# Optimization experiments

Measured on AMD Instinct MI355X. Metric: run time of the kernel, lower is better.

## Reference

```python
import jax, jax.numpy as jnp
import numpy as np

COMMITMENT_COST = 0.25

def _conv(x, w, stride, pad):
    return jax.lax.conv_general_dilated(
        x, w, window_strides=(stride, stride),
        padding=((pad, pad), (pad, pad)),
        dimension_numbers=("NCHW", "OIHW", "NCHW"))

def _gelu(x):
    return jax.nn.gelu(x, approximate=False)

def setup_inputs() -> dict:
    key = jax.random.key(0)
    ks = jax.random.split(key, 9)
    def w(k, shape):
        fan_in = shape[1] * shape[2] * shape[3]
        return jax.random.normal(k, shape, jnp.float32) / jnp.sqrt(fan_in)
    return {
        "x": jax.random.normal(ks[0], (32, 3, 256, 256), jnp.float32),
        "enc_w1": w(ks[1], (64, 3, 5, 5)),
        "enc_w2": w(ks[2], (64, 64, 5, 5)),
        "enc_w3": w(ks[3], (64, 64, 2, 2)),
        "dec_w1": w(ks[4], (512, 64, 2, 2)),
        "dec_w2": w(ks[5], (256, 512, 2, 2)),
        "dec_w3": w(ks[6], (256, 256, 2, 2)),
        "codes": jax.random.normal(ks[7], (24, 64), jnp.float32),
        "ema_count": jax.random.uniform(ks[8], (24,), jnp.float32) + 0.1,
    }

def reference(x, enc_w1, enc_w2, enc_w3, dec_w1, dec_w2, dec_w3, codes, ema_count):
    # ---- encoder: 256 -> 128 -> 64 -> 63, channels 3 -> 64 ----
    z = _conv(x, enc_w1, 2, 2)
    z = _gelu(z)
    z = _conv(z, enc_w2, 2, 2)
    z = _gelu(z)
    z = _conv(z, enc_w3, 1, 0)          # [B, 64, 63, 63]

    # ---- VQ codebook (EMA variant: commitment loss only) ----
    B, C, H, W = z.shape
    zf = jnp.transpose(z, (0, 2, 3, 1)).reshape(-1, C)          # [N, C]
    # squared L2 distances to each code
    d = (jnp.sum(zf * zf, axis=1, keepdims=True)
         - 2.0 * zf @ codes.T
         + jnp.sum(codes * codes, axis=1))                       # [N, K]
    idx = jnp.argmin(d, axis=1)                                  # [N]
    zq = codes[idx].reshape(B, H, W, C).transpose(0, 3, 1, 2)    # [B, C, H, W]

    vq_loss = COMMITMENT_COST * jnp.mean(
        (jax.lax.stop_gradient(zq) - z) ** 2)
    # straight-through estimator
    z_hat = z + jax.lax.stop_gradient(zq - z)

    # code probabilities from EMA cluster counts, gathered per position
    probs = ema_count / jnp.sum(ema_count)                       # [K]
    z_probs = probs[idx].reshape(B, H, W)                        # [B, H, W]

    # ---- decoder: 63 -> 64 -> 63 -> 64, channels 64 -> 512 -> 256 -> 256 ----
    y = _conv(z_hat, dec_w1, 1, 1)
    y = _gelu(y)
    y = _conv(y, dec_w2, 1, 0)
    y = _gelu(y)
    x_hat = _conv(y, dec_w3, 1, 1)      # [B, 256, 64, 64]

    return (x_hat, z_probs, vq_loss)
```

## Files before the change

kernel.cpp:

```cpp
#include <hip/hip_runtime.h>
#include <hip/hip_bf16.h>


#define DEV_INLINE __device__ __forceinline__

typedef __attribute__((ext_vector_type(8))) short bf16x8;
typedef __attribute__((ext_vector_type(4))) float f32x4;

#define GLL16(g, l) __builtin_amdgcn_global_load_lds(                      \
    (const __attribute__((address_space(1))) void*)(g),                    \
    (__attribute__((address_space(3))) void*)(l), 16, 0, 0)

DEV_INLINE float gelu_exact(float v) {
    return 0.5f * v * (1.0f + erff(v * 0.70710678118654752440f));
}

__global__ void wtf_k(const float* __restrict__ w, float* __restrict__ wt,
                      int C, int total) {
    int t = blockIdx.x * 256 + threadIdx.x;
    if (t >= total) return;
    int oc = t & 63;
    int rest = t >> 6;
    int tap = rest % 25, c = rest / 25;
    wt[t] = w[(oc * C + c) * 25 + tap];
}

template<int C, int IH, int IW>
__global__ __launch_bounds__(256) void conv5s2_t(
    const float* __restrict__ xg,
    const float* __restrict__ wt,
    float* __restrict__ outg) {
    constexpr int OH = IH / 2, OW = IW / 2;
    __shared__ float xin[35 * 36];
    __shared__ float wl[1600];
    const int tid = threadIdx.x;
    const int n = blockIdx.z;
    const int OY0 = blockIdx.y * 16, OX0 = blockIdx.x * 16;
    const int IY0 = OY0 * 2 - 2, IX0 = OX0 * 2 - 2;
    const int og = tid & 3;
    const int pg = tid >> 2;
    const int py = (pg >> 3) * 2, px = (pg & 7) * 2;
    const int ry = py * 2, rx = px * 2;

    f32x4 a00 = {0,0,0,0}, a01 = a00, a02 = a00, a03 = a00;
    f32x4 a10 = a00, a11 = a00, a12 = a00, a13 = a00;
    f32x4 a20 = a00, a21 = a00, a22 = a00, a23 = a00;
    f32x4 a30 = a00, a31 = a00, a32 = a00, a33 = a00;

    const float* xn = xg + (size_t)n * C * IH * IW;
    for (int c = 0; c < C; ++c) {
        {
            const float4* wsrc = (const float4*)(wt + c * 1600);
            float4* wdst = (float4*)wl;
            wdst[tid] = wsrc[tid];
            if (tid < 144) wdst[256 + tid] = wsrc[256 + tid];
        }
        const float* zc = xn + (size_t)c * IH * IW;
        for (int i = tid; i < 1225; i += 256) {
            int r = i / 35, cl = i - r * 35;
            int iy = IY0 + r, ix = IX0 + cl;
            float v = 0.f;
            if ((unsigned)iy < (unsigned)IH && (unsigned)ix < (unsigned)IW)
                v = zc[(size_t)iy * IW + ix];
            xin[r * 36 + cl] = v;
        }
        __syncthreads();
#pragma unroll
        for (int ky = 0; ky < 5; ++ky) {
            const float* r0 = xin + (ry + ky) * 36 + rx;
            const float* r1 = r0 + 72;
#pragma unroll
            for (int kx = 0; kx < 5; ++kx) {
                const f32x4* wq = (const f32x4*)(wl + (ky * 5 + kx) * 64 + og * 16);
                f32x4 w0 = wq[0], w1 = wq[1], w2 = wq[2], w3 = wq[3];
                float xA = r0[kx], xB = r0[kx + 2];
                float xC = r1[kx], xD = r1[kx + 2];
                a00 += xA * w0; a01 += xA * w1; a02 += xA * w2; a03 += xA * w3;
                a10 += xB * w0; a11 += xB * w1; a12 += xB * w2; a13 += xB * w3;
                a20 += xC * w0; a21 += xC * w1; a22 += xC * w2; a23 += xC * w3;
                a30 += xD * w0; a31 += xD * w1; a32 += xD * w2; a33 += xD * w3;
            }
        }
        __syncthreads();
    }
    const int ocb = og * 16;
#define CSTORE(v, oy, ox, q) {                                                \
        float* o = outg + (((size_t)n * 64 + ocb + (q) * 4) * OH + (oy)) * OW \
                   + (ox);                                                    \
        o[0]               = gelu_exact((v).x);                               \
        o[(size_t)OH * OW]     = gelu_exact((v).y);                           \
        o[(size_t)2 * OH * OW] = gelu_exact((v).z);                           \
        o[(size_t)3 * OH * OW] = gelu_exact((v).w); }
    CSTORE(a00, OY0 + py,     OX0 + px,     0); CSTORE(a01, OY0 + py,     OX0 + px,     1);
    CSTORE(a02, OY0 + py,     OX0 + px,     2); CSTORE(a03, OY0 + py,     OX0 + px,     3);
    CSTORE(a10, OY0 + py,     OX0 + px + 1, 0); CSTORE(a11, OY0 + py,     OX0 + px + 1, 1);
    CSTORE(a12, OY0 + py,     OX0 + px + 1, 2); CSTORE(a13, OY0 + py,     OX0 + px + 1, 3);
    CSTORE(a20, OY0 + py + 1, OX0 + px,     0); CSTORE(a21, OY0 + py + 1, OX0 + px,     1);
    CSTORE(a22, OY0 + py + 1, OX0 + px,     2); CSTORE(a23, OY0 + py + 1, OX0 + px,     3);
    CSTORE(a30, OY0 + py + 1, OX0 + px + 1, 0); CSTORE(a31, OY0 + py + 1, OX0 + px + 1, 1);
    CSTORE(a32, OY0 + py + 1, OX0 + px + 1, 2); CSTORE(a33, OY0 + py + 1, OX0 + px + 1, 3);
#undef CSTORE
}

template<int C, int IH, int IW>
__global__ __launch_bounds__(256) void conv5s2_p(
    const float* __restrict__ xg,
    const float* __restrict__ wt,
    float* __restrict__ outg) {
    constexpr int OH = IH / 2, OW = IW / 2;
    __shared__ float xp[2 * 700];
    __shared__ float wl[1600];
    const int tid = threadIdx.x;
    const int n = blockIdx.z;
    const int OY0 = blockIdx.y * 16, OX0 = blockIdx.x * 16;
    const int IY0 = OY0 * 2 - 2, IX0 = OX0 * 2 - 2;
    const int og = tid & 7;
    const int pg = tid >> 3;
    const int py = (pg >> 2) * 2, px = (pg & 3) * 4;
    const int ry = py * 2;
    const int s4 = og & 4;

    f32x4 a000 = {0,0,0,0}, a001 = a000, a010 = a000, a011 = a000;
    f32x4 a020 = a000, a021 = a000, a030 = a000, a031 = a000;
    f32x4 a100 = a000, a101 = a000, a110 = a000, a111 = a000;
    f32x4 a120 = a000, a121 = a000, a130 = a000, a131 = a000;

    const float* xn = xg + (size_t)n * C * IH * IW;
    for (int c = 0; c < C; ++c) {
        {
            const float4* wsrc = (const float4*)(wt + c * 1600);
            float4* wdst = (float4*)wl;
            wdst[tid ^ ((tid >> 3) & 1)] = wsrc[tid];
            if (tid < 144) {
                int i2 = 256 + tid;
                wdst[i2 ^ ((i2 >> 3) & 1)] = wsrc[i2];
            }
        }
        const float* zc = xn + (size_t)c * IH * IW;
        for (int i = tid; i < 1225; i += 256) {
            int r = i / 35, cl = i - r * 35;
            int iy = IY0 + r, ix = IX0 + cl;
            float v = 0.f;
            if ((unsigned)iy < (unsigned)IH && (unsigned)ix < (unsigned)IW)
                v = zc[(size_t)iy * IW + ix];
            xp[(cl & 1) * 700 + r * 20 + (cl >> 1)] = v;
        }
        __syncthreads();

#define PICK8(Ea, Eb, i) ((i) < 4 ? (Ea)[(i) & 3] : (Eb)[(i) & 3])
#define XV(R, kx, jj) (((kx) & 1)                                           \
        ? PICK8(O##R##0, O##R##1, (jj) + ((kx) >> 1))                       \
        : PICK8(E##R##0, E##R##1, (jj) + ((kx) >> 1)))

#pragma unroll
        for (int ky = 0; ky < 5; ++ky) {
            const int R0 = ry + ky;
            const int R1 = R0 + 2;
            const f32x4 E00 = *(const f32x4*)(xp + R0 * 20 + px);
            const f32x4 E01 = *(const f32x4*)(xp + R0 * 20 + px + 4);
            const f32x4 O00 = *(const f32x4*)(xp + 700 + R0 * 20 + px);
            const f32x4 O01 = *(const f32x4*)(xp + 700 + R0 * 20 + px + 4);
            const f32x4 E10 = *(const f32x4*)(xp + R1 * 20 + px);
            const f32x4 E11 = *(const f32x4*)(xp + R1 * 20 + px + 4);
            const f32x4 O10 = *(const f32x4*)(xp + 700 + R1 * 20 + px);
            const f32x4 O11 = *(const f32x4*)(xp + 700 + R1 * 20 + px + 4);
#pragma unroll
            for (int kx = 0; kx < 5; ++kx) {
                const float* wb = wl + (ky * 5 + kx) * 64 + og * 8;
                f32x4 w0 = *(const f32x4*)(wb + s4);
                f32x4 w1 = *(const f32x4*)(wb + (s4 ^ 4));
                float xA = XV(0, kx, 0), xB = XV(0, kx, 1);
                float xC = XV(0, kx, 2), xD = XV(0, kx, 3);
                float xE = XV(1, kx, 0), xF = XV(1, kx, 1);
                float xG = XV(1, kx, 2), xH = XV(1, kx, 3);
                a000 += xA * w0; a001 += xA * w1;
                a010 += xB * w0; a011 += xB * w1;
                a020 += xC * w0; a021 += xC * w1;
                a030 += xD * w0; a031 += xD * w1;
                a100 += xE * w0; a101 += xE * w1;
                a110 += xF * w0; a111 += xF * w1;
                a120 += xG * w0; a121 += xG * w1;
                a130 += xH * w0; a131 += xH * w1;
            }
        }
#undef XV
#undef PICK8
        __syncthreads();
    }

    const size_t HW = (size_t)OH * OW;
#define STR(q, vA, vB, vC, vD, vE, vF, vG, vH) {                           \
        _Pragma("unroll")                                                  \
        for (int j = 0; j < 4; ++j) {                                      \
            float* o = outg + ((size_t)n * 64 + og * 8 + (q) * 4 + j) * HW \
                       + (size_t)(OY0 + py) * OW + (OX0 + px);             \
            f32x4 t0, t1;                                                  \
            t0[0] = gelu_exact((vA)[j]); t0[1] = gelu_exact((vB)[j]);      \
            t0[2] = gelu_exact((vC)[j]); t0[3] = gelu_exact((vD)[j]);      \
            t1[0] = gelu_exact((vE)[j]); t1[1] = gelu_exact((vF)[j]);      \
            t1[2] = gelu_exact((vG)[j]); t1[3] = gelu_exact((vH)[j]);      \
            *(f32x4*)o = t0;                                               \
            *(f32x4*)(o + OW) = t1;                                        \
        } }
    STR(0, a000, a010, a020, a030, a100, a110, a120, a130)
    STR(1, a001, a011, a021, a031, a101, a111, a121, a131)
#undef STR
}

__global__ void conv3_k(const float* __restrict__ z2,
                        const float* __restrict__ w,
                        float* __restrict__ z) {
    __shared__ float wl[1024];
    const int oc0 = blockIdx.y * 4;
    for (int i = threadIdx.x; i < 1024; i += 256) {
        int j = i & 3, r = i >> 2;
        wl[i] = w[(oc0 + j) * 256 + r];
    }
    __syncthreads();
    const int s = blockIdx.x * 256 + threadIdx.x;
    if (s >= 3969) return;
    const int n = blockIdx.z;
    const int oy = s / 63, ox = s % 63;
    const float4* wv = (const float4*)wl;
    float a0 = 0.f, a1 = 0.f, a2 = 0.f, a3 = 0.f;
    const float* zn = z2 + n * 64 * 4096;
    for (int c = 0; c < 64; ++c) {
        const float* zc = zn + c * 4096;
#pragma unroll
        for (int tap = 0; tap < 4; ++tap) {
            int iy = oy + (tap >> 1), ix = ox + (tap & 1);
            float xv = zc[iy * 64 + ix];
            float4 wq = wv[c * 4 + tap];
            a0 += xv * wq.x; a1 += xv * wq.y; a2 += xv * wq.z; a3 += xv * wq.w;
        }
    }
    int obase = (n * 64 + oc0) * 3969 + s;
    z[obase]            = a0;
    z[obase + 3969]     = a1;
    z[obase + 2 * 3969] = a2;
    z[obase + 3 * 3969] = a3;
}

__global__ void vq_k(const float* __restrict__ z,
                     const float* __restrict__ codes,
                     const float* __restrict__ ema,
                     int* __restrict__ idxO,
                     float* __restrict__ zprobsO,
                     float* __restrict__ lossO) {
    __shared__ float cl[1536];
    __shared__ float cn[24];
    __shared__ float pr[24];
    for (int i = threadIdx.x; i < 1536; i += 256) cl[i] = codes[i];
    if (threadIdx.x < 24) pr[threadIdx.x] = ema[threadIdx.x];
    __syncthreads();
    if (threadIdx.x < 24) {
        float sm = 0.f;
        for (int c = 0; c < 64; ++c) { float v = cl[threadIdx.x * 64 + c]; sm += v * v; }
        cn[threadIdx.x] = sm;
    }
    __syncthreads();
    int t = blockIdx.x * 256 + threadIdx.x;
    float l = 0.f;
    if (t < 127008) {
        int b = t / 3969, s = t - b * 3969;
        const float* zp = z + (b * 64) * 3969 + s;
        float zv[64];
        float zn = 0.f;
#pragma unroll
        for (int c = 0; c < 64; ++c) { float v = zp[c * 3969]; zv[c] = v; zn += v * v; }
        float best = 1e30f; int bi = 0;
        for (int k = 0; k < 24; ++k) {
            float dot = 0.f;
#pragma unroll
            for (int c = 0; c < 64; ++c) dot += zv[c] * cl[k * 64 + c];
            float d = zn - 2.f * dot + cn[k];
            if (d < best) { best = d; bi = k; }
        }
        idxO[t] = bi;
        float psum = 0.f;
        for (int k = 0; k < 24; ++k) psum += pr[k];
        zprobsO[t] = pr[bi] / psum;
        for (int c = 0; c < 64; ++c) { float dd = cl[bi * 64 + c] - zv[c]; l += dd * dd; }
    }
    for (int off = 32; off; off >>= 1) l += __shfl_down(l, off, 64);
    if ((threadIdx.x & 63) == 0) atomicAdd(lossO, l);
}

__global__ void dtab_k(const float* __restrict__ codes,
                       const float* __restrict__ w1,
                       float* __restrict__ D) {
    int t = blockIdx.x * 256 + threadIdx.x;
    if (t >= 24 * 4 * 512) return;
    int oc = t & 511, tap = (t >> 9) & 3, k = t >> 11;
    float acc = 0.f;
    for (int c = 0; c < 64; ++c)
        acc += codes[k * 64 + c] * w1[oc * 256 + c * 4 + tap];
    D[t] = acc;
}

__global__ void wt_k(const float* __restrict__ w, __hip_bfloat16* __restrict__ wT,
                     int cl2, int total) {
    int t = blockIdx.x * 256 + threadIdx.x;
    if (t >= total) return;
    int c = t & ((1 << cl2) - 1);
    int tap = (t >> cl2) & 3;
    int oc = t >> (cl2 + 2);
    wT[t] = __float2bfloat16(w[((oc << cl2) + c) * 4 + tap]);
}

__global__ void dec1_k(const int* __restrict__ idx,
                       const float* __restrict__ D,
                       __hip_bfloat16* __restrict__ y1) {
    const int pos = blockIdx.x;
    const int n = pos >> 12, rem = pos & 4095;
    const int iy = rem >> 6, ix = rem & 63;
    const int* idn = idx + n * 3969;
    const int t = threadIdx.x;
    float ax = 0.f, ay = 0.f;
#pragma unroll
    for (int tap = 0; tap < 4; ++tap) {
        int py = iy - 1 + (tap >> 1), px = ix - 1 + (tap & 1);
        if ((unsigned)py < 63u && (unsigned)px < 63u) {
            int k = idn[py * 63 + px];
            float2 v = ((const float2*)(D + (k * 4 + tap) * 512))[t];
            ax += v.x; ay += v.y;
        }
    }
    __hip_bfloat162 o;
    o.x = __float2bfloat16(gelu_exact(ax));
    o.y = __float2bfloat16(gelu_exact(ay));
    ((__hip_bfloat162*)(y1 + (size_t)pos * 512))[t] = o;
}

__global__ __launch_bounds__(256) void dec2_mfma(
    const __hip_bfloat16* __restrict__ y1,
    const __hip_bfloat16* __restrict__ wT,
    const __hip_bfloat16* __restrict__ zp,
    __hip_bfloat16* __restrict__ y2)
{
    __shared__ __hip_bfloat16 As[128 * 32];
    __shared__ __hip_bfloat16 Bs[128 * 32];
    const int tid = threadIdx.x;
    const int wave = tid >> 6, lane = tid & 63;
    const int quad = lane >> 4, l15 = lane & 15;
    const int m0 = blockIdx.x * 128;
    const int oc0 = blockIdx.y * 128;
    const int sub = tid & 3;

    const char* pA[2];
    const char* pB[2];
#pragma unroll
    for (int j = 0; j < 2; ++j) {
        int slot = j * 64 + (tid >> 2);
        int pp = m0 + slot;
        if (pp < 127008) {
            int n = pp / 3969; int r = pp - n * 3969;
            int oy = r / 63;  int ox = r - oy * 63;
            pA[j] = (const char*)y1 + (size_t)((n * 64 + oy) * 64 + ox) * 1024 + sub * 16;
        } else {
            pA[j] = (const char*)zp;
        }
        pB[j] = (const char*)wT + (size_t)(oc0 + slot) * 4096 + sub * 16;
    }
    char* ldsA[2] = {(char*)As + wave * 1024, (char*)As + 4096 + wave * 1024};
    char* ldsB[2] = {(char*)Bs + wave * 1024, (char*)Bs + 4096 + wave * 1024};

    f32x4 acc[4][4] = {};
    const int wm = (wave & 1) * 64;
    const int wn = (wave >> 1) * 64;

#pragma unroll
    for (int tap = 0; tap < 4; ++tap) {
        const int toff = ((tap >> 1) * 64 + (tap & 1)) * 1024;
        for (int kk = 0; kk < 16; ++kk) {
            const int cb = kk * 64;
            GLL16(pA[0] + toff + cb, ldsA[0]);
            GLL16(pA[1] + toff + cb, ldsA[1]);
            GLL16(pB[0] + tap * 1024 + cb, ldsB[0]);
            GLL16(pB[1] + tap * 1024 + cb, ldsB[1]);
            __syncthreads();
            bf16x8 af[4], bf[4];
#pragma unroll
            for (int mi = 0; mi < 4; ++mi)
                af[mi] = *(const bf16x8*)((const char*)As + (wm + mi * 16 + l15) * 64 + quad * 16);
#pragma unroll
            for (int ni = 0; ni < 4; ++ni)
                bf[ni] = *(const bf16x8*)((const char*)Bs + (wn + ni * 16 + l15) * 64 + quad * 16);
#pragma unroll
            for (int mi = 0; mi < 4; ++mi)
#pragma unroll
                for (int ni = 0; ni < 4; ++ni)
                    acc[mi][ni] = __builtin_amdgcn_mfma_f32_16x16x32_bf16(
                        af[mi], bf[ni], acc[mi][ni], 0, 0, 0);
            __syncthreads();
        }
    }
#pragma unroll
    for (int mi = 0; mi < 4; ++mi)
#pragma unroll
        for (int r = 0; r < 4; ++r) {
            int pos = m0 + wm + mi * 16 + quad * 4 + r;
            if (pos < 127008) {
#pragma unroll
                for (int ni = 0; ni < 4; ++ni) {
                    int oc = oc0 + wn + ni * 16 + l15;
                    y2[(size_t)pos * 256 + oc] =
                        __float2bfloat16(gelu_exact(acc[mi][ni][r]));
                }
            }
        }
}

__global__ __launch_bounds__(256) void dec3_mfma(
    const __hip_bfloat16* __restrict__ y2,
    const __hip_bfloat16* __restrict__ wT,
    const __hip_bfloat16* __restrict__ zp,
    float* __restrict__ out)
{
    __shared__ __hip_bfloat16 As[128 * 32];
    __shared__ __hip_bfloat16 Bs[128 * 32];
    const int tid = threadIdx.x;
    const int wave = tid >> 6, lane = tid & 63;
    const int quad = lane >> 4, l15 = lane & 15;
    const int p0 = blockIdx.x * 128;
    const int oc0 = blockIdx.y * 128;
    const int sub = tid & 3;

    const char* pW[2];
    const char* pP[4][2];
#pragma unroll
    for (int j = 0; j < 2; ++j) {
        int slot = j * 64 + (tid >> 2);
        pW[j] = (const char*)wT + (size_t)(oc0 + slot) * 2048 + sub * 16;
        int pp = p0 + slot;
        int n = pp >> 12, rem = pp & 4095;
        int OY = rem >> 6, OX = rem & 63;
#pragma unroll
        for (int tap = 0; tap < 4; ++tap) {
            int iy = OY - 1 + (tap >> 1), ix = OX - 1 + (tap & 1);
            if ((unsigned)iy < 63u && (unsigned)ix < 63u)
                pP[tap][j] = (const char*)y2 + (size_t)(n * 3969 + iy * 63 + ix) * 512 + sub * 16;
            else
                pP[tap][j] = (const char*)zp;
        }
    }
    char* ldsA[2] = {(char*)As + wave * 1024, (char*)As + 4096 + wave * 1024};
    char* ldsB[2] = {(char*)Bs + wave * 1024, (char*)Bs + 4096 + wave * 1024};

    f32x4 acc[4][4] = {};
    const int wm = (wave & 1) * 64;
    const int wn = (wave >> 1) * 64;

#pragma unroll
    for (int tap = 0; tap < 4; ++tap) {
        for (int kk = 0; kk < 8; ++kk) {
            const int cb = kk * 64;
            GLL16(pW[0] + tap * 512 + cb, ldsA[0]);
            GLL16(pW[1] + tap * 512 + cb, ldsA[1]);
            GLL16(pP[tap][0] + cb, ldsB[0]);
            GLL16(pP[tap][1] + cb, ldsB[1]);
            __syncthreads();
            bf16x8 af[4], bf[4];
#pragma unroll
            for (int mi = 0; mi < 4; ++mi)
                af[mi] = *(const bf16x8*)((const char*)As + (wm + mi * 16 + l15) * 64 + quad * 16);
#pragma unroll
            for (int ni = 0; ni < 4; ++ni)
                bf[ni] = *(const bf16x8*)((const char*)Bs + (wn + ni * 16 + l15) * 64 + quad * 16);
#pragma unroll
            for (int mi = 0; mi < 4; ++mi)
#pragma unroll
                for (int ni = 0; ni < 4; ++ni)
                    acc[mi][ni] = __builtin_amdgcn_mfma_f32_16x16x32_bf16(
                        af[mi], bf[ni], acc[mi][ni], 0, 0, 0);
            __syncthreads();
        }
    }
    const int n = p0 >> 12;
    const int posLocal0 = (p0 & 4095) + wn;
#pragma unroll
    for (int mi = 0; mi < 4; ++mi)
#pragma unroll
        for (int r = 0; r < 4; ++r) {
            int oc = oc0 + wm + mi * 16 + quad * 4 + r;
            float* orow = out + ((size_t)(n * 256 + oc) << 12);
#pragma unroll
            for (int ni = 0; ni < 4; ++ni)
                orow[posLocal0 + ni * 16 + l15] = acc[mi][ni][r];
        }
}

__global__ void loss_k(const float* __restrict__ lossO, float* __restrict__ out) {
    out[0] = 0.25f * lossO[0] / 8128512.0f;
}

extern "C" void kernel_launch(void* const* d_in, const int* in_sizes, int n_in,
                              void* d_out, int out_size, void* d_ws, size_t ws_size,
                              hipStream_t stream) {
    const float* x     = (const float*)d_in[0];
    const float* ew1   = (const float*)d_in[1];
    const float* ew2   = (const float*)d_in[2];
    const float* ew3   = (const float*)d_in[3];
    const float* dw1   = (const float*)d_in[4];
    const float* dw2   = (const float*)d_in[5];
    const float* dw3   = (const float*)d_in[6];
    const float* codes = (const float*)d_in[7];
    const float* ema   = (const float*)d_in[8];
    float* out = (float*)d_out;

    char* ws = (char*)d_ws;
    float* z1   = (float*)(ws + 0);
    float* z2   = (float*)(ws + 134217728);
    float* z    = (float*)(ws + 167772160);
    int*   idx  = (int*)  (ws + 200286208);
    float* loss = (float*)(ws + 200794240);
    __hip_bfloat16* zp  = (__hip_bfloat16*)(ws + 200794496);
    float* D    = (float*)(ws + 200864128);
    __hip_bfloat16* wT2 = (__hip_bfloat16*)(ws + 201650560);
    __hip_bfloat16* wT3 = (__hip_bfloat16*)(ws + 202699136);
    float* wt2f = (float*)(ws + 201650560);
    float* wt1f = (float*)(ws + 202699136);
    __hip_bfloat16* y1  = (__hip_bfloat16*)(ws + 0);
    __hip_bfloat16* y2  = (__hip_bfloat16*)(ws + 134217728);

    hipMemsetAsync(loss, 0, 4, stream);
    hipMemsetAsync(zp, 0, 69632, stream);

    wtf_k<<<dim3(19), 256, 0, stream>>>(ew1, wt1f, 3, 4800);
    wtf_k<<<dim3(400), 256, 0, stream>>>(ew2, wt2f, 64, 102400);
    conv5s2_t<3, 256, 256><<<dim3(8, 8, 32), 256, 0, stream>>>(x, wt1f, z1);
    conv5s2_p<64, 128, 128><<<dim3(4, 4, 32), 256, 0, stream>>>(z1, wt2f, z2);
    conv3_k<<<dim3(16, 16, 32), 256, 0, stream>>>(z2, ew3, z);
    vq_k<<<dim3(497), 256, 0, stream>>>(z, codes, ema, idx, out + 33554432, loss);
    dtab_k<<<dim3(192), 256, 0, stream>>>(codes, dw1, D);
    wt_k<<<dim3(2048), 256, 0, stream>>>(dw2, wT2, 9, 524288);
    wt_k<<<dim3(1024), 256, 0, stream>>>(dw3, wT3, 8, 262144);
    dec1_k<<<dim3(131072), 256, 0, stream>>>(idx, D, y1);
    dec2_mfma<<<dim3(993, 2), 256, 0, stream>>>(y1, wT2, zp, y2);
    dec3_mfma<<<dim3(1024, 2), 256, 0, stream>>>(y2, wT3, zp, out);
    loss_k<<<1, 1, 0, stream>>>(loss, out + 33681440);
}
```

Measured before the change: 1.209 ms.

## Double-buffer input and weight tiles in second encoder conv with register prefetch

The second 5x5 stride-2 encoder convolution now keeps two LDS buffers for input patches and weights. It prefetches the next channel's data into registers while computing the current channel, then writes it to the other buffer, so each channel needs one barrier instead of two. Interior tiles use vectorised float2 loads with precomputed offsets in place of per-element bounds checks. This costs double the shared memory, a launch bound that allows one block per SM, and more registers held across the compute loop.

Result: slower. 1.268 ms (+4.8%).

```diff
diff --git a/kernel.cpp b/kernel.cpp
--- a/kernel.cpp
+++ b/kernel.cpp
@@ -103,13 +103,13 @@
 }
 
 template<int C, int IH, int IW>
-__global__ __launch_bounds__(256) void conv5s2_p(
+__global__ __launch_bounds__(256, 1) void conv5s2_p2(
     const float* __restrict__ xg,
     const float* __restrict__ wt,
     float* __restrict__ outg) {
     constexpr int OH = IH / 2, OW = IW / 2;
-    __shared__ float xp[2 * 700];
-    __shared__ float wl[1600];
+    __shared__ float xp[2][1400];
+    __shared__ float wl[2][1600];
     const int tid = threadIdx.x;
     const int n = blockIdx.z;
     const int OY0 = blockIdx.y * 16, OX0 = blockIdx.x * 16;
@@ -120,53 +120,118 @@
     const int ry = py * 2;
     const int s4 = og & 4;
 
+    const bool interior = (IY0 >= 0) && (IY0 + 35 <= IH) &&
+                          (IX0 >= 0) && (IX0 + 36 <= IW);
+
+    const bool hasB = (tid < 59);
+    const int rA = tid / 9,         qA = tid - rA * 9;
+    const int sB = 256 + tid;
+    const int rB = sB / 9,          qB = sB - rB * 9;
+    int gA0, gA1, gA2, gA3, gB0 = 0, gB1 = 0, gB2 = 0, gB3 = 0;
+    int bA0, bA1, bA2, bA3, bB0 = 0, bB1 = 0, bB2 = 0, bB3 = 0;
+    {
+        int iy = IY0 + rA; int rok = ((unsigned)iy < (unsigned)IH);
+        int ixb = IX0 + 4 * qA; int base = iy * IW + ixb;
+        bA0 = rok && ((unsigned)(ixb)     < (unsigned)IW); gA0 = bA0 ? base     : 0;
+        bA1 = rok && ((unsigned)(ixb + 1) < (unsigned)IW); gA1 = bA1 ? base + 1 : 0;
+        bA2 = rok && ((unsigned)(ixb + 2) < (unsigned)IW); gA2 = bA2 ? base + 2 : 0;
+        bA3 = rok && ((unsigned)(ixb + 3) < (unsigned)IW); gA3 = bA3 ? base + 3 : 0;
+        if (interior) gA0 = base;
+    }
+    if (hasB) {
+        int iy = IY0 + rB; int rok = ((unsigned)iy < (unsigned)IH);
+        int ixb = IX0 + 4 * qB; int base = iy * IW + ixb;
+        bB0 = rok && ((unsigned)(ixb)     < (unsigned)IW); gB0 = bB0 ? base     : 0;
+        bB1 = rok && ((unsigned)(ixb + 1) < (unsigned)IW); gB1 = bB1 ? base + 1 : 0;
+        bB2 = rok && ((unsigned)(ixb + 2) < (unsigned)IW); gB2 = bB2 ? base + 2 : 0;
+        bB3 = rok && ((unsigned)(ixb + 3) < (unsigned)IW); gB3 = bB3 ? base + 3 : 0;
+        if (interior) gB0 = base;
+    }
+    const int eA = rA * 20 + 2 * qA;
+    const int eB = rB * 20 + 2 * qB;
+    const int swA = tid ^ ((tid >> 3) & 1);
+    const int iw2 = 256 + tid;
+    const int swB = iw2 ^ ((iw2 >> 3) & 1);
+
+    const float* xn = xg + (size_t)n * C * IH * IW;
+
+    f32x4 vA = {0,0,0,0}, vB = {0,0,0,0};
+    float4 wgA = {0,0,0,0}, wgB = {0,0,0,0};
+
+#define SLOAD(cc) {                                                         \
+        const float* zc = xn + (size_t)(cc) * IH * IW;                      \
+        if (interior) {                                                     \
+            const float2* pa = (const float2*)(zc + gA0);                   \
+            float2 a0 = pa[0], a1 = pa[1];                                  \
+            vA[0] = a0.x; vA[1] = a0.y; vA[2] = a1.x; vA[3] = a1.y;         \
+            if (hasB) {                                                     \
+                const float2* pb = (const float2*)(zc + gB0);               \
+                float2 b0 = pb[0], b1 = pb[1];                              \
+                vB[0] = b0.x; vB[1] = b0.y; vB[2] = b1.x; vB[3] = b1.y;     \
+            }                                                               \
+        } else {                                                            \
+            vA[0] = bA0 ? zc[gA0] : 0.f; vA[1] = bA1 ? zc[gA1] : 0.f;       \
+            vA[2] = bA2 ? zc[gA2] : 0.f; vA[3] = bA3 ? zc[gA3] : 0.f;       \
+            if (hasB) {                                                     \
+                vB[0] = bB0 ? zc[gB0] : 0.f; vB[1] = bB1 ? zc[gB1] : 0.f;   \
+                vB[2] = bB2 ? zc[gB2] : 0.f; vB[3] = bB3 ? zc[gB3] : 0.f;   \
+            }                                                               \
+        }                                                                   \
+        const float4* ws = (const float4*)(wt + (size_t)(cc) * 1600);       \
+        wgA = ws[tid];                                                      \
+        if (tid < 144) wgB = ws[256 + tid]; }
+
+#define SWRITE(nb) {                                                        \
+        float* xw = xp[nb];                                                 \
+        float2 tE, tO;                                                      \
+        tE.x = vA[0]; tE.y = vA[2];                                         \
+        tO.x = vA[1]; tO.y = vA[3];                                         \
+        *(float2*)(xw + eA) = tE;                                           \
+        *(float2*)(xw + 700 + eA) = tO;                                     \
+        if (hasB) {                                                         \
+            tE.x = vB[0]; tE.y = vB[2];                                     \
+            tO.x = vB[1]; tO.y = vB[3];                                     \
+            *(float2*)(xw + eB) = tE;                                       \
+            *(float2*)(xw + 700 + eB) = tO;                                 \
+        }                                                                   \
+        float4* wd = (float4*)wl[nb];                                       \
+        wd[swA] = wgA;                                                      \
+        if (tid < 144) wd[swB] = wgB; }
+
     f32x4 a000 = {0,0,0,0}, a001 = a000, a010 = a000, a011 = a000;
     f32x4 a020 = a000, a021 = a000, a030 = a000, a031 = a000;
     f32x4 a100 = a000, a101 = a000, a110 = a000, a111 = a000;
     f32x4 a120 = a000, a121 = a000, a130 = a000, a131 = a000;
 
-    const float* xn = xg + (size_t)n * C * IH * IW;
+    SLOAD(0)
+    SWRITE(0)
+    __syncthreads();
+
     for (int c = 0; c < C; ++c) {
-        {
-            const float4* wsrc = (const float4*)(wt + c * 1600);
-            float4* wdst = (float4*)wl;
-            wdst[tid ^ ((tid >> 3) & 1)] = wsrc[tid];
-            if (tid < 144) {
-                int i2 = 256 + tid;
-                wdst[i2 ^ ((i2 >> 3) & 1)] = wsrc[i2];
-            }
-        }
-        const float* zc = xn + (size_t)c * IH * IW;
-        for (int i = tid; i < 1225; i += 256) {
-            int r = i / 35, cl = i - r * 35;
-            int iy = IY0 + r, ix = IX0 + cl;
-            float v = 0.f;
-            if ((unsigned)iy < (unsigned)IH && (unsigned)ix < (unsigned)IW)
-                v = zc[(size_t)iy * IW + ix];
-            xp[(cl & 1) * 700 + r * 20 + (cl >> 1)] = v;
-        }
-        __syncthreads();
+        const int bf = c & 1;
+        if (c + 1 < C) SLOAD(c + 1)
+        const float* xb = xp[bf];
+        const float* wbs = wl[bf];
 
 #define PICK8(Ea, Eb, i) ((i) < 4 ? (Ea)[(i) & 3] : (Eb)[(i) & 3])
 #define XV(R, kx, jj) (((kx) & 1)                                           \
         ? PICK8(O##R##0, O##R##1, (jj) + ((kx) >> 1))                       \
         : PICK8(E##R##0, E##R##1, (jj) + ((kx) >> 1)))
-
 #pragma unroll
         for (int ky = 0; ky < 5; ++ky) {
             const int R0 = ry + ky;
             const int R1 = R0 + 2;
-            const f32x4 E00 = *(const f32x4*)(xp + R0 * 20 + px);
-            const f32x4 E01 = *(const f32x4*)(xp + R0 * 20 + px + 4);
-            const f32x4 O00 = *(const f32x4*)(xp + 700 + R0 * 20 + px);
-            const f32x4 O01 = *(const f32x4*)(xp + 700 + R0 * 20 + px + 4);
-            const f32x4 E10 = *(const f32x4*)(xp + R1 * 20 + px);
-            const f32x4 E11 = *(const f32x4*)(xp + R1 * 20 + px + 4);
-            const f32x4 O10 = *(const f32x4*)(xp + 700 + R1 * 20 + px);
-            const f32x4 O11 = *(const f32x4*)(xp + 700 + R1 * 20 + px + 4);
+            const f32x4 E00 = *(const f32x4*)(xb + R0 * 20 + px);
+            const f32x4 E01 = *(const f32x4*)(xb + R0 * 20 + px + 4);
+            const f32x4 O00 = *(const f32x4*)(xb + 700 + R0 * 20 + px);
+            const f32x4 O01 = *(const f32x4*)(xb + 700 + R0 * 20 + px + 4);
+            const f32x4 E10 = *(const f32x4*)(xb + R1 * 20 + px);
+            const f32x4 E11 = *(const f32x4*)(xb + R1 * 20 + px + 4);
+            const f32x4 O10 = *(const f32x4*)(xb + 700 + R1 * 20 + px);
+            const f32x4 O11 = *(const f32x4*)(xb + 700 + R1 * 20 + px + 4);
 #pragma unroll
             for (int kx = 0; kx < 5; ++kx) {
-                const float* wb = wl + (ky * 5 + kx) * 64 + og * 8;
+                const float* wb = wbs + (ky * 5 + kx) * 64 + og * 8;
                 f32x4 w0 = *(const f32x4*)(wb + s4);
                 f32x4 w1 = *(const f32x4*)(wb + (s4 ^ 4));
                 float xA = XV(0, kx, 0), xB = XV(0, kx, 1);
@@ -185,20 +250,25 @@
         }
 #undef XV
 #undef PICK8
-        __syncthreads();
-    }
+        if (c + 1 < C) {
+            SWRITE(bf ^ 1)
+            __syncthreads();
+        }
+    }
+#undef SLOAD
+#undef SWRITE
 
     const size_t HW = (size_t)OH * OW;
-#define STR(q, vA, vB, vC, vD, vE, vF, vG, vH) {                           \
+#define STR(q, vA_, vB_, vC_, vD_, vE_, vF_, vG_, vH_) {                   \
         _Pragma("unroll")                                                  \
         for (int j = 0; j < 4; ++j) {                                      \
             float* o = outg + ((size_t)n * 64 + og * 8 + (q) * 4 + j) * HW \
                        + (size_t)(OY0 + py) * OW + (OX0 + px);             \
             f32x4 t0, t1;                                                  \
-            t0[0] = gelu_exact((vA)[j]); t0[1] = gelu_exact((vB)[j]);      \
-            t0[2] = gelu_exact((vC)[j]); t0[3] = gelu_exact((vD)[j]);      \
-            t1[0] = gelu_exact((vE)[j]); t1[1] = gelu_exact((vF)[j]);      \
-            t1[2] = gelu_exact((vG)[j]); t1[3] = gelu_exact((vH)[j]);      \
+            t0[0] = gelu_exact((vA_)[j]); t0[1] = gelu_exact((vB_)[j]);    \
+            t0[2] = gelu_exact((vC_)[j]); t0[3] = gelu_exact((vD_)[j]);    \
+            t1[0] = gelu_exact((vE_)[j]); t1[1] = gelu_exact((vF_)[j]);    \
+            t1[2] = gelu_exact((vG_)[j]); t1[3] = gelu_exact((vH_)[j]);    \
             *(f32x4*)o = t0;                                               \
             *(f32x4*)(o + OW) = t1;                                        \
         } }
@@ -529,7 +599,7 @@
     wtf_k<<<dim3(19), 256, 0, stream>>>(ew1, wt1f, 3, 4800);
     wtf_k<<<dim3(400), 256, 0, stream>>>(ew2, wt2f, 64, 102400);
     conv5s2_t<3, 256, 256><<<dim3(8, 8, 32), 256, 0, stream>>>(x, wt1f, z1);
-    conv5s2_p<64, 128, 128><<<dim3(4, 4, 32), 256, 0, stream>>>(z1, wt2f, z2);
+    conv5s2_p2<64, 128, 128><<<dim3(4, 4, 32), 256, 0, stream>>>(z1, wt2f, z2);
     conv3_k<<<dim3(16, 16, 32), 256, 0, stream>>>(z2, ew3, z);
     vq_k<<<dim3(497), 256, 0, stream>>>(z, codes, ema, idx, out + 33554432, loss);
     dtab_k<<<dim3(192), 256, 0, stream>>>(codes, dw1, D);
```
